# Performance work log

Measured on AMD Instinct MI355X. Metric: run time of the kernel, lower is better.

## Reference

```python
import jax, jax.numpy as jnp
import numpy as np

N_HEADS = 4
D_HEAD = 32  # out_features // n_heads = 128 // 4
NEG_SLOPE = 0.2


def setup_inputs() -> dict:
    key = jax.random.key(0)
    k_x, k_adj, k_w, k_a = jax.random.split(key, 4)
    B, N, F_in, F_out = 4, 2048, 128, 128
    x = jax.random.normal(k_x, (B, N, F_in), dtype=jnp.float32)
    adj = jax.random.randint(k_adj, (B, N, N), 0, 2, dtype=jnp.int32)
    # Linear weight stored as [in, out] (torch stores [out, in]; math identical: x @ W)
    w_scale = np.sqrt(2.0 / (F_in + F_out))  # xavier-ish
    W = jax.random.normal(k_w, (F_in, F_out), dtype=jnp.float32) * w_scale
    a = jax.random.normal(k_a, (N_HEADS, 2 * D_HEAD), dtype=jnp.float32) * np.sqrt(2.0 / (2 * D_HEAD))
    return {"x": x, "adj": adj, "W": W, "a": a}


def reference(x, adj, W, a):
    B, N, _ = x.shape
    # project and split heads: [B, H, N, D]
    h = jnp.einsum('bnf,fo->bno', x, W).reshape(B, N, N_HEADS, D_HEAD).transpose(0, 2, 1, 3)
    # additive attention logits
    e_src = jnp.einsum('bhnd,hd->bhn', h, a[:, :D_HEAD])  # [B,H,N]
    e_dst = jnp.einsum('bhnd,hd->bhn', h, a[:, D_HEAD:])  # [B,H,N]
    e = e_src[:, :, :, None] + e_dst[:, :, None, :]       # [B,H,N,N]
    e = jnp.where(e > 0, e, NEG_SLOPE * e)                # leaky_relu(0.2)
    mask = (adj[:, None, :, :] == 0)                      # [B,1,N,N] -> broadcast over heads
    e = jnp.where(mask, -jnp.inf, e)
    alpha = jax.nn.softmax(e, axis=-1)                    # dropout omitted (eval mode)
    out = jnp.einsum('bhnm,bhmd->bhnd', alpha, h)         # weighted aggregation
    out = out.transpose(0, 2, 1, 3).reshape(B, N, N_HEADS * D_HEAD)
    return jax.nn.elu(out)
```

## Files before the change

kernel.cpp:

```cpp
#include <hip/hip_runtime.h>
#include <hip/hip_bf16.h>

#define BB 4
#define NN 2048
#define FIN 128
#define NH 4
#define DH 32
#define NS 0.2f

typedef unsigned int u32;
typedef unsigned short u16;
typedef unsigned long long u64;
typedef __attribute__((ext_vector_type(8))) short short8;
typedef __attribute__((ext_vector_type(4))) float f32x4;
typedef __attribute__((ext_vector_type(4))) unsigned int u32x4;

#define OFF_ES 0
#define OFF_ED 32768
#define OFF_PQ 65536
#define OFF_M  131072
#define OFF_HT 131088
#define OFF_BITS 655376

__device__ __forceinline__ u16 f2bf_rne(float f) {
  unsigned u = __float_as_uint(f);
  return (u16)((u + 0x7fffu + ((u >> 16) & 1u)) >> 16);
}

__global__ __launch_bounds__(256) void k_pack(const int* __restrict__ adj,
                                              u32* __restrict__ bits) {
  const int row = (blockIdx.x << 2) | (threadIdx.x >> 6);
  const int lane = threadIdx.x & 63;
  const int* src = adj + (size_t)row * NN;
  u32* dst = bits + (size_t)row * 64;
#pragma unroll 8
  for (int it = 0; it < 32; ++it) {
    const int v = src[it * 64 + lane];
    const u64 m = __ballot(v != 0);
    if (lane == 0) *(u64*)(dst + it * 2) = m;
  }
}

__global__ __launch_bounds__(256) void k_proj(
    const float* __restrict__ x, const float* __restrict__ W,
    const float* __restrict__ a, u16* __restrict__ hT,
    float* __restrict__ e_src, float* __restrict__ e_dst) {
  __shared__ float Ws[FIN * 128];
  const int tid = threadIdx.x;
  const int f = tid & 127, g = tid >> 7;
  const float4* Wg4 = (const float4*)W;
  float4* Ws4 = (float4*)Ws;
#pragma unroll
  for (int t = 0; t < 16; ++t) Ws4[t * 256 + tid] = Wg4[t * 256 + tid];
  __syncthreads();

  const int rb = blockIdx.x * 16 + g * 8;
  const int head = f >> 5, d = f & 31;
  const int b = rb >> 11, n0 = rb & (NN - 1);
  const int bh = b * NH + head;
  const float a_s = a[head * (2 * DH) + d];
  const float a_d = a[head * (2 * DH) + DH + d];

  float acc[8];
#pragma unroll
  for (int r = 0; r < 8; ++r) acc[r] = 0.f;

  const float* xb = x + (size_t)rb * FIN;
  for (int k = 0; k < FIN; ++k) {
    const float wv = Ws[k * 128 + f];
#pragma unroll
    for (int r = 0; r < 8; ++r) acc[r] = fmaf(wv, xb[r * FIN + k], acc[r]);
  }

  u16 hs[8];
#pragma unroll
  for (int r = 0; r < 8; ++r) hs[r] = f2bf_rne(acc[r]);
  u16* dst = hT + ((size_t)bh * DH + d) * NN + n0;
  *(int4*)dst = *(int4*)&hs[0];

#pragma unroll
  for (int r = 0; r < 8; ++r) {
    float s1 = acc[r] * a_s;
    float s2 = acc[r] * a_d;
#pragma unroll
    for (int off = 16; off >= 1; off >>= 1) {
      s1 += __shfl_xor(s1, off);
      s2 += __shfl_xor(s2, off);
    }
    if (d == 0) {
      e_src[(size_t)bh * NN + n0 + r] = s1;
      e_dst[(size_t)bh * NN + n0 + r] = s2;
    }
  }
}

__global__ __launch_bounds__(64) void k_prep(
    const float* __restrict__ e_dst, u32* __restrict__ PQ,
    float* __restrict__ M) {
  const int bh = blockIdx.x >> 3, seg = blockIdx.x & 7;
  const int lane = threadIdx.x;
  const float* ed = e_dst + (size_t)bh * NN;
  float m = -1e30f;
#pragma unroll
  for (int t = 0; t < 32; ++t) m = fmaxf(m, ed[t * 64 + lane]);
#pragma unroll
  for (int off = 32; off >= 1; off >>= 1) m = fmaxf(m, __shfl_xor(m, off));
  if (seg == 0 && lane == 0) M[bh] = m;
#pragma unroll
  for (int t = 0; t < 4; ++t) {
    const int j = seg * 256 + t * 64 + lane;
    const float e = ed[j];
    const u32 pb = f2bf_rne(__expf(e));
    const u32 qb = f2bf_rne(__expf(NS * e));
    PQ[(size_t)bh * NN + j] = (qb << 16) | pb;
  }
}

__global__ __launch_bounds__(256) void k_attn(
    const u16* __restrict__ hT, const float* __restrict__ e_src,
    const u32* __restrict__ PQv, const float* __restrict__ Mv,
    const u32* __restrict__ bits, float* __restrict__ out) {
  __shared__ __align__(16) u16 smem[4][2][32 * 64];

  const int bid = blockIdx.x;
  const int bh = bid >> 6;
  const int it = bid & 63;
  const int b = bh >> 2, head = bh & 3;

  const int w = threadIdx.x >> 6;
  const int lane = threadIdx.x & 63;
  const int lg = lane >> 4, lm = lane & 15;

  const int i0 = it * 32 + lm;
  const int i1 = i0 + 16;
  const float m = Mv[bh];
  const float es0 = e_src[(size_t)bh * NN + i0];
  const float es1 = e_src[(size_t)bh * NN + i1];
  const float mr0 = es0 + m, mr1 = es1 + m;
  const float mi0 = fmaxf(mr0, NS * mr0), mi1 = fmaxf(mr1, NS * mr1);
  const float A0 = __expf(es0 - mi0), B0 = __expf(NS * es0 - mi0);
  const float A1 = __expf(es1 - mi1), B1 = __expf(NS * es1 - mi1);

  const u32* PQb = PQv + (size_t)bh * NN + w * 512;
  const u16* hb = hT + (size_t)bh * DH * NN + w * 512;
  const u32* br0 = bits + ((size_t)b * NN + i0) * 64 + w * 16;
  const u32* br1 = bits + ((size_t)b * NN + i1) * 64 + w * 16;
  const int shamt = lg * 8;

  const int sd = lane >> 3;
  const int sj = (lane & 7) * 8;
  u16* stg0 = &smem[w][0][0];
  u16* stg1 = &smem[w][1][0];
  const int woff = (sd * 64 + sj) ^ (sd << 3);

  f32x4 acc00 = {0,0,0,0}, acc01 = {0,0,0,0};
  f32x4 acc10 = {0,0,0,0}, acc11 = {0,0,0,0};
  float S0 = 0.f, S1 = 0.f;

  {
    int4 r0 = *(const int4*)(hb + (size_t)(0 * 8 + sd) * NN + sj);
    int4 r1 = *(const int4*)(hb + (size_t)(1 * 8 + sd) * NN + sj);
    int4 r2 = *(const int4*)(hb + (size_t)(2 * 8 + sd) * NN + sj);
    int4 r3 = *(const int4*)(hb + (size_t)(3 * 8 + sd) * NN + sj);
    *(int4*)(stg0 + woff) = r0;
    *(int4*)(stg0 + woff + 1 * 512) = r1;
    *(int4*)(stg0 + woff + 2 * 512) = r2;
    *(int4*)(stg0 + woff + 3 * 512) = r3;
  }

  const int ra0 = (lm * 64) ^ ((lm & 7) << 3);

#pragma unroll
  for (int s = 0; s < 8; ++s) {
    u16* cur = (s & 1) ? stg1 : stg0;
    u16* nxt = (s & 1) ? stg0 : stg1;
    int4 n0, n1, n2, n3;
    if (s < 7) {
      const u16* g = hb + (s + 1) * 64;
      n0 = *(const int4*)(g + (size_t)(0 * 8 + sd) * NN + sj);
      n1 = *(const int4*)(g + (size_t)(1 * 8 + sd) * NN + sj);
      n2 = *(const int4*)(g + (size_t)(2 * 8 + sd) * NN + sj);
      n3 = *(const int4*)(g + (size_t)(3 * 8 + sd) * NN + sj);
    }
    const u64 wb0 = *(const u64*)(br0 + s * 2);
    const u64 wb1 = *(const u64*)(br1 + s * 2);
#pragma unroll
    for (int c = 0; c < 2; ++c) {
      const int jl = c * 32 + lg * 8;
      const u32x4 pqa = *(const u32x4*)(PQb + s * 64 + jl);
      const u32x4 pqb = *(const u32x4*)(PQb + s * 64 + jl + 4);
      const short8 hv0 = *(const short8*)(cur + (ra0 ^ jl));
      const short8 hv1 = *(const short8*)(cur + ((ra0 ^ jl) + 16 * 64));
      const u32 wsh0 = ((u32)(wb0 >> (c * 32))) >> shamt;
      const u32 wsh1 = ((u32)(wb1 >> (c * 32))) >> shamt;
      short8 af0, af1;
#pragma unroll
      for (int e = 0; e < 8; ++e) {
        const u32 pq = (e < 4) ? pqa[e] : pqb[e - 4];
        const float Pf = __uint_as_float(pq << 16);
        const float Qf = __uint_as_float(pq & 0xffff0000u);
        const int m0 = ((int)(wsh0 << (31 - e))) >> 31;
        const int m1 = ((int)(wsh1 << (31 - e))) >> 31;
        float w0 = fmaxf(A0 * Pf, B0 * Qf);
        w0 = __int_as_float(__float_as_int(w0) & m0);
        S0 += w0;
        af0[e] = (short)__builtin_bit_cast(unsigned short, __float2bfloat16(w0));
        float w1 = fmaxf(A1 * Pf, B1 * Qf);
        w1 = __int_as_float(__float_as_int(w1) & m1);
        S1 += w1;
        af1[e] = (short)__builtin_bit_cast(unsigned short, __float2bfloat16(w1));
      }
      __builtin_amdgcn_s_setprio(1);
      acc00 = __builtin_amdgcn_mfma_f32_16x16x32_bf16(af0, hv0, acc00, 0, 0, 0);
      acc01 = __builtin_amdgcn_mfma_f32_16x16x32_bf16(af0, hv1, acc01, 0, 0, 0);
      acc10 = __builtin_amdgcn_mfma_f32_16x16x32_bf16(af1, hv0, acc10, 0, 0, 0);
      acc11 = __builtin_amdgcn_mfma_f32_16x16x32_bf16(af1, hv1, acc11, 0, 0, 0);
      __builtin_amdgcn_s_setprio(0);
    }
    if (s < 7) {
      *(int4*)(nxt + woff) = n0;
      *(int4*)(nxt + woff + 1 * 512) = n1;
      *(int4*)(nxt + woff + 2 * 512) = n2;
      *(int4*)(nxt + woff + 3 * 512) = n3;
    }
  }

  S0 += __shfl_xor(S0, 16); S0 += __shfl_xor(S0, 32);
  S1 += __shfl_xor(S1, 16); S1 += __shfl_xor(S1, 32);

  __syncthreads();
  float (*part)[32][33] = (float (*)[32][33]) & smem[0][0][0];
  float (*sp)[2][16] = (float (*)[2][16])((char*)&smem[0][0][0] + 16896);

#pragma unroll
  for (int r = 0; r < 4; ++r) {
    const int rl = lg * 4 + r;
    part[w][rl][lm] = acc00[r];
    part[w][rl][16 + lm] = acc01[r];
    part[w][16 + rl][lm] = acc10[r];
    part[w][16 + rl][16 + lm] = acc11[r];
  }
  if (lg == 0) { sp[w][0][lm] = S0; sp[w][1][lm] = S1; }
  __syncthreads();

  const int tid = threadIdx.x;
#pragma unroll
  for (int t = 0; t < 4; ++t) {
    const int idx = t * 256 + tid;
    const int row = idx >> 5, d = idx & 31;
    const float v = part[0][row][d] + part[1][row][d] +
                    part[2][row][d] + part[3][row][d];
    const float s = sp[0][row >> 4][row & 15] + sp[1][row >> 4][row & 15] +
                    sp[2][row >> 4][row & 15] + sp[3][row >> 4][row & 15];
    const float o = v / s;
    const int n = it * 32 + row;
    out[((size_t)b * NN + n) * 128 + head * 32 + d] =
        o > 0.f ? o : (__expf(o) - 1.f);
  }
}

extern "C" void kernel_launch(void* const* d_in, const int* in_sizes, int n_in,
                              void* d_out, int out_size, void* d_ws, size_t ws_size,
                              hipStream_t stream) {
  const float* x = (const float*)d_in[0];
  const int* adj = (const int*)d_in[1];
  const float* W = (const float*)d_in[2];
  const float* a = (const float*)d_in[3];
  float* out = (float*)d_out;
  float* ws = (float*)d_ws;

  float* e_src = ws + OFF_ES;
  float* e_dst = ws + OFF_ED;
  u32* PQv = (u32*)(ws + OFF_PQ);
  float* Mv = ws + OFF_M;
  u16* hT = (u16*)(ws + OFF_HT);
  u32* bits = (u32*)(ws + OFF_BITS);

  k_pack<<<(BB * NN) / 4, 256, 0, stream>>>(adj, bits);
  k_proj<<<(BB * NN) / 16, 256, 0, stream>>>(x, W, a, hT, e_src, e_dst);
  k_prep<<<BB * NH * 8, 64, 0, stream>>>(e_dst, PQv, Mv);
  k_attn<<<BB * NH * 64, 256, 0, stream>>>(hT, e_src, PQv, Mv, bits, out);
}
```

Measured before the change: 62.43 us.

## Prefetch PQ and mask bits one step ahead; sum weights via MFMA with ones

Loads the next step's packed P/Q values and adjacency bitmask words into registers during the current step, so global latency overlaps the compute loop. Replaces the per-element scalar accumulation of softmax denominators with two extra MFMAs against a bf16 ones vector, which frees VALU work but sums bf16-rounded weights rather than fp32 weights. Mask extraction uses a signed bitfield-extract builtin when available. Risks more register pressure from the prefetch buffers and a small change in numerical behaviour.

```diff
diff --git a/kernel.cpp b/kernel.cpp
--- a/kernel.cpp
+++ b/kernel.cpp
@@ -25,6 +25,14 @@
 __device__ __forceinline__ u16 f2bf_rne(float f) {
   unsigned u = __float_as_uint(f);
   return (u16)((u + 0x7fffu + ((u >> 16) & 1u)) >> 16);
+}
+
+__device__ __forceinline__ int bitmask(u32 w, int e) {
+#if __has_builtin(__builtin_amdgcn_sbfe)
+  return __builtin_amdgcn_sbfe((int)w, e, 1);
+#else
+  return ((int)(w << (31 - e))) >> 31;
+#endif
 }
 
 __global__ __launch_bounds__(256) void k_pack(const int* __restrict__ adj,
@@ -146,6 +154,7 @@
   const u32* br0 = bits + ((size_t)b * NN + i0) * 64 + w * 16;
   const u32* br1 = bits + ((size_t)b * NN + i1) * 64 + w * 16;
   const int shamt = lg * 8;
+  const int jb = lg * 8;
 
   const int sd = lane >> 3;
   const int sj = (lane & 7) * 8;
@@ -153,9 +162,13 @@
   u16* stg1 = &smem[w][1][0];
   const int woff = (sd * 64 + sj) ^ (sd << 3);
 
+  short8 ones;
+#pragma unroll
+  for (int e = 0; e < 8; ++e) ones[e] = (short)0x3F80;
+
   f32x4 acc00 = {0,0,0,0}, acc01 = {0,0,0,0};
   f32x4 acc10 = {0,0,0,0}, acc11 = {0,0,0,0};
-  float S0 = 0.f, S1 = 0.f;
+  f32x4 accS0 = {0,0,0,0}, accS1 = {0,0,0,0};
 
   {
     int4 r0 = *(const int4*)(hb + (size_t)(0 * 8 + sd) * NN + sj);
@@ -167,6 +180,12 @@
     *(int4*)(stg0 + woff + 2 * 512) = r2;
     *(int4*)(stg0 + woff + 3 * 512) = r3;
   }
+  u32x4 pqa0_c = *(const u32x4*)(PQb + jb);
+  u32x4 pqb0_c = *(const u32x4*)(PQb + jb + 4);
+  u32x4 pqa1_c = *(const u32x4*)(PQb + 32 + jb);
+  u32x4 pqb1_c = *(const u32x4*)(PQb + 32 + jb + 4);
+  u64 wb0_c = *(const u64*)(br0);
+  u64 wb1_c = *(const u64*)(br1);
 
   const int ra0 = (lm * 64) ^ ((lm & 7) << 3);
 
@@ -175,39 +194,44 @@
     u16* cur = (s & 1) ? stg1 : stg0;
     u16* nxt = (s & 1) ? stg0 : stg1;
     int4 n0, n1, n2, n3;
+    u32x4 pqa0_n, pqb0_n, pqa1_n, pqb1_n;
+    u64 wb0_n, wb1_n;
     if (s < 7) {
       const u16* g = hb + (s + 1) * 64;
       n0 = *(const int4*)(g + (size_t)(0 * 8 + sd) * NN + sj);
       n1 = *(const int4*)(g + (size_t)(1 * 8 + sd) * NN + sj);
       n2 = *(const int4*)(g + (size_t)(2 * 8 + sd) * NN + sj);
       n3 = *(const int4*)(g + (size_t)(3 * 8 + sd) * NN + sj);
-    }
-    const u64 wb0 = *(const u64*)(br0 + s * 2);
-    const u64 wb1 = *(const u64*)(br1 + s * 2);
+      const u32* pqn = PQb + (s + 1) * 64;
+      pqa0_n = *(const u32x4*)(pqn + jb);
+      pqb0_n = *(const u32x4*)(pqn + jb + 4);
+      pqa1_n = *(const u32x4*)(pqn + 32 + jb);
+      pqb1_n = *(const u32x4*)(pqn + 32 + jb + 4);
+      wb0_n = *(const u64*)(br0 + (s + 1) * 2);
+      wb1_n = *(const u64*)(br1 + (s + 1) * 2);
+    }
 #pragma unroll
     for (int c = 0; c < 2; ++c) {
-      const int jl = c * 32 + lg * 8;
-      const u32x4 pqa = *(const u32x4*)(PQb + s * 64 + jl);
-      const u32x4 pqb = *(const u32x4*)(PQb + s * 64 + jl + 4);
+      const int jl = c * 32 + jb;
+      const u32x4 pqa = c ? pqa1_c : pqa0_c;
+      const u32x4 pqb = c ? pqb1_c : pqb0_c;
       const short8 hv0 = *(const short8*)(cur + (ra0 ^ jl));
       const short8 hv1 = *(const short8*)(cur + ((ra0 ^ jl) + 16 * 64));
-      const u32 wsh0 = ((u32)(wb0 >> (c * 32))) >> shamt;
-      const u32 wsh1 = ((u32)(wb1 >> (c * 32))) >> shamt;
+      const u32 wsh0 = ((u32)(wb0_c >> (c * 32))) >> shamt;
+      const u32 wsh1 = ((u32)(wb1_c >> (c * 32))) >> shamt;
       short8 af0, af1;
 #pragma unroll
       for (int e = 0; e < 8; ++e) {
         const u32 pq = (e < 4) ? pqa[e] : pqb[e - 4];
         const float Pf = __uint_as_float(pq << 16);
         const float Qf = __uint_as_float(pq & 0xffff0000u);
-        const int m0 = ((int)(wsh0 << (31 - e))) >> 31;
-        const int m1 = ((int)(wsh1 << (31 - e))) >> 31;
+        const int m0 = bitmask(wsh0, e);
+        const int m1 = bitmask(wsh1, e);
         float w0 = fmaxf(A0 * Pf, B0 * Qf);
         w0 = __int_as_float(__float_as_int(w0) & m0);
-        S0 += w0;
         af0[e] = (short)__builtin_bit_cast(unsigned short, __float2bfloat16(w0));
         float w1 = fmaxf(A1 * Pf, B1 * Qf);
         w1 = __int_as_float(__float_as_int(w1) & m1);
-        S1 += w1;
         af1[e] = (short)__builtin_bit_cast(unsigned short, __float2bfloat16(w1));
       }
       __builtin_amdgcn_s_setprio(1);
@@ -215,6 +239,8 @@
       acc01 = __builtin_amdgcn_mfma_f32_16x16x32_bf16(af0, hv1, acc01, 0, 0, 0);
       acc10 = __builtin_amdgcn_mfma_f32_16x16x32_bf16(af1, hv0, acc10, 0, 0, 0);
       acc11 = __builtin_amdgcn_mfma_f32_16x16x32_bf16(af1, hv1, acc11, 0, 0, 0);
+      accS0 = __builtin_amdgcn_mfma_f32_16x16x32_bf16(af0, ones, accS0, 0, 0, 0);
+      accS1 = __builtin_amdgcn_mfma_f32_16x16x32_bf16(af1, ones, accS1, 0, 0, 0);
       __builtin_amdgcn_s_setprio(0);
     }
     if (s < 7) {
@@ -222,11 +248,11 @@
       *(int4*)(nxt + woff + 1 * 512) = n1;
       *(int4*)(nxt + woff + 2 * 512) = n2;
       *(int4*)(nxt + woff + 3 * 512) = n3;
-    }
-  }
-
-  S0 += __shfl_xor(S0, 16); S0 += __shfl_xor(S0, 32);
-  S1 += __shfl_xor(S1, 16); S1 += __shfl_xor(S1, 32);
+      pqa0_c = pqa0_n; pqb0_c = pqb0_n;
+      pqa1_c = pqa1_n; pqb1_c = pqb1_n;
+      wb0_c = wb0_n; wb1_c = wb1_n;
+    }
+  }
 
   __syncthreads();
   float (*part)[32][33] = (float (*)[32][33]) & smem[0][0][0];
@@ -240,7 +266,13 @@
     part[w][16 + rl][lm] = acc10[r];
     part[w][16 + rl][16 + lm] = acc11[r];
   }
-  if (lg == 0) { sp[w][0][lm] = S0; sp[w][1][lm] = S1; }
+  if (lm == 0) {
+#pragma unroll
+    for (int r = 0; r < 4; ++r) {
+      sp[w][0][lg * 4 + r] = accS0[r];
+      sp[w][1][lg * 4 + r] = accS1[r];
+    }
+  }
   __syncthreads();
 
   const int tid = threadIdx.x;
```

Result: no change. 62.72 us (+0.5%).
